# Optimization experiments

Hardware: AMD Instinct MI355X
Metric: run time of the kernel (lower is better)

The kernel has to match this reference:

```python
import jax, jax.numpy as jnp
import numpy as np
from functools import partial

U = 1200   # thought_size (GRU units)
E = 620    # word_size
V = 20000  # vocab_size
B = 128    # batch
T = 64     # seq_len
LN_EPS = 1e-3  # Keras LayerNormalization default epsilon


def layernorm(x, gamma, beta, eps=LN_EPS):
    m = jnp.mean(x, axis=-1, keepdims=True)
    v = jnp.mean(jnp.square(x - m), axis=-1, keepdims=True)
    return gamma * (x - m) * jax.lax.rsqrt(v + eps) + beta


def gru_ln_direction(emb, kernel, rkernel, bias, ln0_g, ln0_b, ln3_g, ln3_b):
    """Run the LayerNorm-GRU (impl=2, reset_after=True) over emb [B,T,E].
    Returns final hidden state [B,U]."""
    input_bias, recurrent_bias = bias[0], bias[1]
    # Time-parallel input projection: [B,T,3U]
    x_proj = jnp.einsum('bte,eu->btu', emb, kernel) + input_bias
    x_proj_t = jnp.transpose(x_proj, (1, 0, 2))  # [T,B,3U]

    def step(h, xt):
        h_ln = layernorm(h, ln0_g, ln0_b)                      # LN on previous state
        inner = h_ln @ rkernel + recurrent_bias                # [B,3U]
        z = jax.nn.sigmoid(xt[:, :U] + inner[:, :U])
        r = jax.nn.sigmoid(xt[:, U:2 * U] + inner[:, U:2 * U])
        rec_h = r * inner[:, 2 * U:]
        hh = jnp.tanh(layernorm(xt[:, 2 * U:] + rec_h, ln3_g, ln3_b))
        h_new = z * h_ln + (1.0 - z) * hh
        return h_new, None

    h0 = jnp.zeros((emb.shape[0], U), dtype=emb.dtype)
    h_final, _ = jax.lax.scan(step, h0, x_proj_t)
    return h_final


def setup_inputs() -> dict:
    key = jax.random.key(0)
    ks = jax.random.split(key, 8)
    s = 0.05
    return {
        'sentences': jax.random.randint(ks[0], (B, T), 0, V),
        'embed': jax.random.normal(ks[1], (V, E), jnp.float32) * s,
        'fw_kernel': jax.random.normal(ks[2], (E, 3 * U), jnp.float32) * s,
        'fw_rkernel': jax.random.normal(ks[3], (U, 3 * U), jnp.float32) * s,
        'fw_bias': jax.random.normal(ks[4], (2, 3 * U), jnp.float32) * s,
        'fw_ln0_g': jnp.ones((U,), jnp.float32),
        'fw_ln0_b': jnp.zeros((U,), jnp.float32),
        'fw_ln3_g': jnp.ones((U,), jnp.float32),
        'fw_ln3_b': jnp.zeros((U,), jnp.float32),
        'bw_kernel': jax.random.normal(ks[5], (E, 3 * U), jnp.float32) * s,
        'bw_rkernel': jax.random.normal(ks[6], (U, 3 * U), jnp.float32) * s,
        'bw_bias': jax.random.normal(ks[7], (2, 3 * U), jnp.float32) * s,
        'bw_ln0_g': jnp.ones((U,), jnp.float32),
        'bw_ln0_b': jnp.zeros((U,), jnp.float32),
        'bw_ln3_g': jnp.ones((U,), jnp.float32),
        'bw_ln3_b': jnp.zeros((U,), jnp.float32),
    }


def reference(sentences, embed, fw_kernel, fw_rkernel, fw_bias,
              fw_ln0_g, fw_ln0_b, fw_ln3_g, fw_ln3_b,
              bw_kernel, bw_rkernel, bw_bias,
              bw_ln0_g, bw_ln0_b, bw_ln3_g, bw_ln3_b):
    embedding = jnp.tanh(embed[sentences])  # [B,T,E]
    forward_h = gru_ln_direction(embedding, fw_kernel, fw_rkernel, fw_bias,
                                 fw_ln0_g, fw_ln0_b, fw_ln3_g, fw_ln3_b)
    backward_h = gru_ln_direction(embedding[:, ::-1, :], bw_kernel, bw_rkernel, bw_bias,
                                  bw_ln0_g, bw_ln0_b, bw_ln3_g, bw_ln3_b)
    thought_vector = jnp.concatenate([forward_h, backward_h], axis=1)  # [B,2U]
    return thought_vector, embedding
```

## Files before the change

kernel.cpp:

```cpp
#include <hip/hip_runtime.h>
#include <hip/hip_bf16.h>

#define U_    1200
#define E_    620
#define B_    128
#define T_    64
#define N3    3600
#define NP    3712
#define KE    640
#define KU    1216
#define WIN   16
#define LN_EPS 1e-3f

#define GBLK  464
#define UBLK  128
#define TBLK  (GBLK + UBLK)

typedef __attribute__((ext_vector_type(8))) short short8;
typedef __attribute__((ext_vector_type(4))) float f32x4;

constexpr size_t OFF_EMBH  = 0;
constexpr size_t SZ_EMB    = (size_t)8192 * KE * 2;
constexpr size_t OFF_EMBL  = OFF_EMBH + SZ_EMB;
constexpr size_t OFF_KTH   = OFF_EMBL + SZ_EMB;
constexpr size_t SZ_KT     = (size_t)2 * NP * KE * 2;
constexpr size_t OFF_KTL   = OFF_KTH + SZ_KT;
constexpr size_t OFF_RKTH  = OFF_KTL + SZ_KT;
constexpr size_t SZ_RKT    = (size_t)2 * NP * KU * 2;
constexpr size_t OFF_RKTL  = OFF_RKTH + SZ_RKT;
constexpr size_t OFF_XPWH  = OFF_RKTL + SZ_RKT;
constexpr size_t SZ_XPW    = (size_t)2 * WIN * B_ * NP * 2;
constexpr size_t OFF_XPWL  = OFF_XPWH + SZ_XPW;
constexpr size_t OFF_INNER = OFF_XPWL + SZ_XPW;
constexpr size_t SZ_INNER  = (size_t)8 * B_ * NP * 4;
constexpr size_t OFF_HLN   = OFF_INNER + SZ_INNER;
constexpr size_t SZ_HLN    = (size_t)2 * B_ * U_ * 4;
constexpr size_t OFF_HLNBH = OFF_HLN + SZ_HLN;
constexpr size_t SZ_HLNB   = (size_t)2 * B_ * KU * 2;
constexpr size_t OFF_HLNBL = OFF_HLNBH + SZ_HLNB;

__device__ inline void lds_load16(const void* g, void* l) {
  __builtin_amdgcn_global_load_lds(
      (const __attribute__((address_space(1))) unsigned int*)g,
      (__attribute__((address_space(3))) unsigned int*)l, 16, 0, 0);
}

__device__ inline float sigmf(float x) { return 1.f / (1.f + expf(-x)); }

__device__ inline int swz_scol(int tid) {
  return (((tid & 7) ^ ((tid >> 3) & 7)) << 3);
}
__device__ inline int swz_off(int row, int kk, int lane) {
  return row * 64 + ((kk * 32 + ((lane >> 4) << 3)) ^ ((row & 7) << 3));
}

__global__ __launch_bounds__(256)
void embed_kernel(const int* __restrict__ sent, const float* __restrict__ embed,
                  float* __restrict__ out_emb,
                  __hip_bfloat16* __restrict__ embH, __hip_bfloat16* __restrict__ embL) {
  const int row = blockIdx.x;
  const int idx = sent[row];
  const float* src = embed + (size_t)idx * E_;
  for (int e = threadIdx.x; e < KE; e += 256) {
    float v = 0.f;
    if (e < E_) {
      v = tanhf(src[e]);
      out_emb[(size_t)row * E_ + e] = v;
    }
    const __hip_bfloat16 hi = __float2bfloat16(v);
    embH[(size_t)row * KE + e] = hi;
    embL[(size_t)row * KE + e] = __float2bfloat16(v - __bfloat162float(hi));
  }
}

__global__ __launch_bounds__(256)
void transpose_cast(const float* __restrict__ W0, const float* __restrict__ W1,
                    __hip_bfloat16* __restrict__ WtHi, __hip_bfloat16* __restrict__ WtLo,
                    int Kreal, int Kp) {
  const int d = blockIdx.z;
  const float* W = d ? W1 : W0;
  __hip_bfloat16* dstH = WtHi + (size_t)d * NP * Kp;
  __hip_bfloat16* dstL = WtLo + (size_t)d * NP * Kp;
  __shared__ float tile[32][33];
  const int n0 = blockIdx.x * 32, k0 = blockIdx.y * 32;
  const int tx = threadIdx.x, ty = threadIdx.y;
#pragma unroll
  for (int i = 0; i < 32; i += 8) {
    const int k = k0 + ty + i, n = n0 + tx;
    tile[ty + i][tx] = (k < Kreal && n < N3) ? W[(size_t)k * N3 + n] : 0.f;
  }
  __syncthreads();
#pragma unroll
  for (int i = 0; i < 32; i += 8) {
    const int n = n0 + ty + i, k = k0 + tx;
    const float v = tile[tx][ty + i];
    const __hip_bfloat16 hi = __float2bfloat16(v);
    dstH[(size_t)n * Kp + k] = hi;
    dstL[(size_t)n * Kp + k] = __float2bfloat16(v - __bfloat162float(hi));
  }
}

__global__ __launch_bounds__(256)
void init_hln(const float* __restrict__ fw_b0, const float* __restrict__ bw_b0,
              float* __restrict__ hln, __hip_bfloat16* __restrict__ hlnbH,
              __hip_bfloat16* __restrict__ hlnbL) {
  const int idx = blockIdx.x * 256 + threadIdx.x;
  if (idx >= 2 * B_ * KU) return;
  const int k = idx % KU;
  const int rowd = idx / KU;
  const int d = rowd >> 7;
  float v = 0.f;
  if (k < U_) {
    v = (d ? bw_b0 : fw_b0)[k];
    hln[(size_t)rowd * U_ + k] = v;
  }
  const __hip_bfloat16 hi = __float2bfloat16(v);
  hlnbH[idx] = hi;
  hlnbL[idx] = __float2bfloat16(v - __bfloat162float(hi));
}

__global__ __launch_bounds__(256)
void xwin_gemm(const __hip_bfloat16* __restrict__ embH, const __hip_bfloat16* __restrict__ embL,
               const __hip_bfloat16* __restrict__ kTH, const __hip_bfloat16* __restrict__ kTL,
               const float* __restrict__ fw_bias, const float* __restrict__ bw_bias,
               __hip_bfloat16* __restrict__ xpwH, __hip_bfloat16* __restrict__ xpwL,
               int w0) {
  constexpr int BM = 128, BN = 128, BK = 64;
  constexpr int WM = 64, WN = 64, FM = 4, FN = 4;
  constexpr int TA = BM * BK, TB = BN * BK;
  const int bid = blockIdx.x;
  const int w = (bid & 7) * 116 + (bid >> 3);
  const int d = w / 464;
  const int q = w % 464;
  const int nt = q / 16, mt = q % 16;
  const int m0 = mt * BM;
  const int n0 = nt * BN;

  const __hip_bfloat16* BH = kTH + (size_t)d * NP * KE;
  const __hip_bfloat16* BL = kTL + (size_t)d * NP * KE;

  const int tid = threadIdx.x;
  const int lane = tid & 63;
  const int wid = tid >> 6;
  const int wr = wid >> 1, wc = wid & 1;

  __shared__ __align__(16) __hip_bfloat16 As[2 * TA];
  __shared__ __align__(16) __hip_bfloat16 Bs[2 * TB];

  f32x4 acc[FM][FN] = {};

  const int srow = tid >> 3;
  const int scol = swz_scol(tid);

  for (int ks = 0; ks < KE / BK; ++ks) {
    const int k0 = ks * BK;
    __syncthreads();
#pragma unroll
    for (int it = 0; it < TA / 2048; ++it) {
      const int row = m0 + it * 32 + srow;
      const int b = row & 127, srel = row >> 7;
      const int txi = d ? (T_ - 1 - (w0 + srel)) : (w0 + srel);
      const size_t goff = (size_t)(b * T_ + txi) * KE + k0 + scol;
      lds_load16(embH + goff, As + it * 2048 + tid * 8);
      lds_load16(embL + goff, As + TA + it * 2048 + tid * 8);
    }
#pragma unroll
    for (int it = 0; it < TB / 2048; ++it) {
      const size_t goff = (size_t)(n0 + it * 32 + srow) * KE + k0 + scol;
      lds_load16(BH + goff, Bs + it * 2048 + tid * 8);
      lds_load16(BL + goff, Bs + TB + it * 2048 + tid * 8);
    }
    __syncthreads();
#pragma unroll
    for (int kk = 0; kk < BK / 32; ++kk) {
      short8 ah[FM], al[FM], bh[FN], bl[FN];
#pragma unroll
      for (int mi = 0; mi < FM; ++mi) {
        const int row = wr * WM + mi * 16 + (lane & 15);
        const int off = swz_off(row, kk, lane);
        ah[mi] = *(const short8*)(As + off);
        al[mi] = *(const short8*)(As + TA + off);
      }
#pragma unroll
      for (int ni = 0; ni < FN; ++ni) {
        const int row = wc * WN + ni * 16 + (lane & 15);
        const int off = swz_off(row, kk, lane);
        bh[ni] = *(const short8*)(Bs + off);
        bl[ni] = *(const short8*)(Bs + TB + off);
      }
#pragma unroll
      for (int mi = 0; mi < FM; ++mi)
#pragma unroll
        for (int ni = 0; ni < FN; ++ni) {
          acc[mi][ni] = __builtin_amdgcn_mfma_f32_16x16x32_bf16(ah[mi], bh[ni], acc[mi][ni], 0, 0, 0);
          acc[mi][ni] = __builtin_amdgcn_mfma_f32_16x16x32_bf16(ah[mi], bl[ni], acc[mi][ni], 0, 0, 0);
          acc[mi][ni] = __builtin_amdgcn_mfma_f32_16x16x32_bf16(al[mi], bh[ni], acc[mi][ni], 0, 0, 0);
        }
    }
  }

  const float* ib = d ? bw_bias : fw_bias;
#pragma unroll
  for (int mi = 0; mi < FM; ++mi)
#pragma unroll
    for (int ni = 0; ni < FN; ++ni) {
      const int gc = n0 + wc * WN + ni * 16 + (lane & 15);
      const float bv = (gc < N3) ? ib[gc] : 0.f;
      const int gr0 = m0 + wr * WM + mi * 16 + ((lane >> 4) << 2);
#pragma unroll
      for (int j = 0; j < 4; ++j) {
        const int gr = gr0 + j;
        const int b = gr & 127, srel = gr >> 7;
        const size_t off = ((size_t)(d * WIN + srel) * B_ + b) * NP + gc;
        const float v = acc[mi][ni][j] + bv;
        const __hip_bfloat16 hi = __float2bfloat16(v);
        xpwH[off] = hi;
        xpwL[off] = __float2bfloat16(v - __bfloat162float(hi));
      }
    }
}

__device__ inline void breduce2(float& a, float& b, float* red, int tid) {
#pragma unroll
  for (int off = 32; off; off >>= 1) {
    a += __shfl_down(a, off, 64);
    b += __shfl_down(b, off, 64);
  }
  const int w = tid >> 6;
  __syncthreads();
  if ((tid & 63) == 0) { red[w] = a; red[4 + w] = b; }
  __syncthreads();
  a = red[0] + red[1] + red[2] + red[3];
  b = red[4] + red[5] + red[6] + red[7];
}

__global__ __launch_bounds__(256)
void step_fused(const __hip_bfloat16* __restrict__ rkTH, const __hip_bfloat16* __restrict__ rkTL,
                __hip_bfloat16* __restrict__ hlnbH, __hip_bfloat16* __restrict__ hlnbL,
                float* __restrict__ hln, float* __restrict__ inner,
                const __hip_bfloat16* __restrict__ xpwH, const __hip_bfloat16* __restrict__ xpwL,
                const float* __restrict__ fw_bias, const float* __restrict__ bw_bias,
                const float* __restrict__ fw_ln0g, const float* __restrict__ fw_ln0b,
                const float* __restrict__ fw_ln3g, const float* __restrict__ fw_ln3b,
                const float* __restrict__ bw_ln0g, const float* __restrict__ bw_ln0b,
                const float* __restrict__ bw_ln3g, const float* __restrict__ bw_ln3b,
                float* __restrict__ out_tv,
                int dG, int doG, int dU, int tU, int doU) {
  __shared__ __align__(16) __hip_bfloat16 As[2][4096];
  __shared__ __align__(16) __hip_bfloat16 Bs[2][4096];
  __shared__ float red[8];

  const int bid = blockIdx.x;
  const int tid = threadIdx.x;

  if (bid < GBLK) {
    if (!doG) return;
    const int x  = bid & 7;
    const int kp = x >> 1;
    const int nh = x & 1;
    const int i  = bid >> 3;
    const int m  = i & 1;
    const int nt = (i >> 1) + 29 * nh;
    const int ks0 = kp * 5;
    const int ks1 = (kp == 3) ? 19 : (ks0 + 5);
    const int m0 = m * 64;
    const int n0 = nt * 64;

    const int lane = tid & 63;
    const int wid = tid >> 6;
    const int wr = wid >> 1, wc = wid & 1;

    const __hip_bfloat16* WH = rkTH + (size_t)dG * NP * KU;
    const __hip_bfloat16* WL = rkTL + (size_t)dG * NP * KU;

    f32x4 acc[2][2] = {};
    const int srow = tid >> 3;
    const int scol = swz_scol(tid);

    for (int ks = ks0; ks < ks1; ++ks) {
      const int k0 = ks * 64;
      __syncthreads();
#pragma unroll
      for (int it = 0; it < 2; ++it) {
        const size_t ga = (size_t)(dG * B_ + m0 + it * 32 + srow) * KU + k0 + scol;
        lds_load16(hlnbH + ga, &As[0][it * 2048 + tid * 8]);
        lds_load16(hlnbL + ga, &As[1][it * 2048 + tid * 8]);
        const size_t gb = (size_t)(n0 + it * 32 + srow) * KU + k0 + scol;
        lds_load16(WH + gb, &Bs[0][it * 2048 + tid * 8]);
        lds_load16(WL + gb, &Bs[1][it * 2048 + tid * 8]);
      }
      __syncthreads();
#pragma unroll
      for (int kk = 0; kk < 2; ++kk) {
        short8 ah[2], al[2], bh[2], bl[2];
#pragma unroll
        for (int mi = 0; mi < 2; ++mi) {
          const int row = wr * 32 + mi * 16 + (lane & 15);
          const int off = swz_off(row, kk, lane);
          ah[mi] = *(const short8*)(&As[0][off]);
          al[mi] = *(const short8*)(&As[1][off]);
        }
#pragma unroll
        for (int nf = 0; nf < 2; ++nf) {
          const int row = wc * 32 + nf * 16 + (lane & 15);
          const int off = swz_off(row, kk, lane);
          bh[nf] = *(const short8*)(&Bs[0][off]);
          bl[nf] = *(const short8*)(&Bs[1][off]);
        }
#pragma unroll
        for (int mi = 0; mi < 2; ++mi)
#pragma unroll
          for (int nf = 0; nf < 2; ++nf) {
            acc[mi][nf] = __builtin_amdgcn_mfma_f32_16x16x32_bf16(ah[mi], bh[nf], acc[mi][nf], 0, 0, 0);
            acc[mi][nf] = __builtin_amdgcn_mfma_f32_16x16x32_bf16(ah[mi], bl[nf], acc[mi][nf], 0, 0, 0);
            acc[mi][nf] = __builtin_amdgcn_mfma_f32_16x16x32_bf16(al[mi], bh[nf], acc[mi][nf], 0, 0, 0);
          }
      }
    }

    float* C = inner + (size_t)(dG * 4 + kp) * B_ * NP;
#pragma unroll
    for (int mi = 0; mi < 2; ++mi)
#pragma unroll
      for (int nf = 0; nf < 2; ++nf) {
        const int gc = n0 + wc * 32 + nf * 16 + (lane & 15);
        const int gr = m0 + wr * 32 + mi * 16 + ((lane >> 4) << 2);
#pragma unroll
        for (int j = 0; j < 4; ++j)
          C[(size_t)(gr + j) * NP + gc] = acc[mi][nf][j];
      }
    return;
  }

  if (!doU) return;
  const int r = bid - GBLK;
  const int d = dU;
  const int srel = tU & (WIN - 1);

  const float* rec0 = inner + ((size_t)(d * 4 + 0) * B_ + r) * NP;
  const float* rec1 = inner + ((size_t)(d * 4 + 1) * B_ + r) * NP;
  const float* rec2 = inner + ((size_t)(d * 4 + 2) * B_ + r) * NP;
  const float* rec3 = inner + ((size_t)(d * 4 + 3) * B_ + r) * NP;
  const size_t xoff = ((size_t)(d * WIN + srel) * B_ + r) * NP;
  const __hip_bfloat16* xH = xpwH + xoff;
  const __hip_bfloat16* xL = xpwL + xoff;
  const float* rb = (d ? bw_bias : fw_bias) + N3;
  const float* g0 = d ? bw_ln0g : fw_ln0g;
  const float* b0 = d ? bw_ln0b : fw_ln0b;
  const float* g3 = d ? bw_ln3g : fw_ln3g;
  const float* b3 = d ? bw_ln3b : fw_ln3b;
  float* hl = hln + ((size_t)d * B_ + r) * U_;
  __hip_bfloat16* hlbH = hlnbH + ((size_t)d * B_ + r) * KU;
  __hip_bfloat16* hlbL = hlnbL + ((size_t)d * B_ + r) * KU;

  float zv[5], cv[5], hv[5];
  float s1 = 0.f, s2 = 0.f;
#pragma unroll
  for (int i = 0; i < 5; ++i) {
    const int c = tid + i * 256;
    if (c < U_) {
      const float xz = __bfloat162float(xH[c]) + __bfloat162float(xL[c]);
      const float xg = __bfloat162float(xH[U_ + c]) + __bfloat162float(xL[U_ + c]);
      const float xh = __bfloat162float(xH[2 * U_ + c]) + __bfloat162float(xL[2 * U_ + c]);
      const float rz = (rec0[c] + rec1[c]) + (rec2[c] + rec3[c]);
      const float rg = (rec0[U_ + c] + rec1[U_ + c]) + (rec2[U_ + c] + rec3[U_ + c]);
      const float rh = (rec0[2 * U_ + c] + rec1[2 * U_ + c]) + (rec2[2 * U_ + c] + rec3[2 * U_ + c]);
      const float z  = sigmf(xz + rz + rb[c]);
      const float rr = sigmf(xg + rg + rb[U_ + c]);
      const float cand = xh + rr * (rh + rb[2 * U_ + c]);
      zv[i] = z; cv[i] = cand;
      s1 += cand; s2 += cand * cand;
    }
  }
  breduce2(s1, s2, red, tid);
  const float m1 = s1 / U_;
  const float is1 = rsqrtf(s2 / U_ - m1 * m1 + LN_EPS);

  float t1 = 0.f, t2 = 0.f;
#pragma unroll
  for (int i = 0; i < 5; ++i) {
    const int c = tid + i * 256;
    if (c < U_) {
      const float hh = tanhf(g3[c] * (cv[i] - m1) * is1 + b3[c]);
      const float hn = zv[i] * hl[c] + (1.f - zv[i]) * hh;
      hv[i] = hn;
      t1 += hn; t2 += hn * hn;
    }
  }
  breduce2(t1, t2, red, tid);
  const float m2 = t1 / U_;
  const float is2 = rsqrtf(t2 / U_ - m2 * m2 + LN_EPS);

#pragma unroll
  for (int i = 0; i < 5; ++i) {
    const int c = tid + i * 256;
    if (c < U_) {
      const float hlnew = g0[c] * (hv[i] - m2) * is2 + b0[c];
      hl[c] = hlnew;
      const __hip_bfloat16 hi = __float2bfloat16(hlnew);
      hlbH[c] = hi;
      hlbL[c] = __float2bfloat16(hlnew - __bfloat162float(hi));
      if (tU == T_ - 1) out_tv[(size_t)r * 2400 + (size_t)d * U_ + c] = hv[i];
    }
  }
}

extern "C" void kernel_launch(void* const* d_in, const int* in_sizes, int n_in,
                              void* d_out, int out_size, void* d_ws, size_t ws_size,
                              hipStream_t stream) {
  const int*   sent      = (const int*)  d_in[0];
  const float* embed     = (const float*)d_in[1];
  const float* fw_kernel = (const float*)d_in[2];
  const float* fw_rkern  = (const float*)d_in[3];
  const float* fw_bias   = (const float*)d_in[4];
  const float* fw_ln0g   = (const float*)d_in[5];
  const float* fw_ln0b   = (const float*)d_in[6];
  const float* fw_ln3g   = (const float*)d_in[7];
  const float* fw_ln3b   = (const float*)d_in[8];
  const float* bw_kernel = (const float*)d_in[9];
  const float* bw_rkern  = (const float*)d_in[10];
  const float* bw_bias   = (const float*)d_in[11];
  const float* bw_ln0g   = (const float*)d_in[12];
  const float* bw_ln0b   = (const float*)d_in[13];
  const float* bw_ln3g   = (const float*)d_in[14];
  const float* bw_ln3b   = (const float*)d_in[15];

  uint8_t* ws = (uint8_t*)d_ws;
  __hip_bfloat16* embH  = (__hip_bfloat16*)(ws + OFF_EMBH);
  __hip_bfloat16* embL  = (__hip_bfloat16*)(ws + OFF_EMBL);
  __hip_bfloat16* kTH   = (__hip_bfloat16*)(ws + OFF_KTH);
  __hip_bfloat16* kTL   = (__hip_bfloat16*)(ws + OFF_KTL);
  __hip_bfloat16* rkTH  = (__hip_bfloat16*)(ws + OFF_RKTH);
  __hip_bfloat16* rkTL  = (__hip_bfloat16*)(ws + OFF_RKTL);
  __hip_bfloat16* xpwH  = (__hip_bfloat16*)(ws + OFF_XPWH);
  __hip_bfloat16* xpwL  = (__hip_bfloat16*)(ws + OFF_XPWL);
  float*          inner = (float*)(ws + OFF_INNER);
  float*          hln   = (float*)(ws + OFF_HLN);
  __hip_bfloat16* hlnbH = (__hip_bfloat16*)(ws + OFF_HLNBH);
  __hip_bfloat16* hlnbL = (__hip_bfloat16*)(ws + OFF_HLNBL);

  float* out_tv  = (float*)d_out;
  float* out_emb = (float*)d_out + (size_t)B_ * 2 * U_;

  embed_kernel<<<B_ * T_, 256, 0, stream>>>(sent, embed, out_emb, embH, embL);

  transpose_cast<<<dim3(NP / 32, KE / 32, 2), dim3(32, 8), 0, stream>>>(
      fw_kernel, bw_kernel, kTH, kTL, E_, KE);
  transpose_cast<<<dim3(NP / 32, KU / 32, 2), dim3(32, 8), 0, stream>>>(
      fw_rkern, bw_rkern, rkTH, rkTL, U_, KU);

  init_hln<<<(2 * B_ * KU + 255) / 256, 256, 0, stream>>>(fw_ln0b, bw_ln0b,
                                                          hln, hlnbH, hlnbL);

#define SF(dG_, doG_, dU_, tU_, doU_)                                          \
  step_fused<<<TBLK, 256, 0, stream>>>(                                        \
      rkTH, rkTL, hlnbH, hlnbL, hln, inner, xpwH, xpwL,                        \
      fw_bias, bw_bias, fw_ln0g, fw_ln0b, fw_ln3g, fw_ln3b,                    \
      bw_ln0g, bw_ln0b, bw_ln3g, bw_ln3b, out_tv,                              \
      dG_, doG_, dU_, tU_, doU_)

  for (int t = 0; t < T_; ++t) {
    SF(0, 1, 1, t - 1, (t > 0) ? 1 : 0);
    if ((t & (WIN - 1)) == 0)
      xwin_gemm<<<928, 256, 0, stream>>>(
          embH, embL, kTH, kTL, fw_bias, bw_bias, xpwH, xpwL, t);
    SF(1, 1, 0, t, 1);
  }
  SF(0, 0, 1, T_ - 1, 1);
#undef SF
}
```

Measured before the change: 2.032 ms.

## Switch recurrent GEMM to fp16 single-weight split and halve K-split blocks

The recurrent weight matrix is now stored as a single fp16 copy instead of bf16 hi/lo pairs, and the hidden state is split into fp16 hi/lo. This cuts MFMAs per tile from three to two and halves the weight bytes loaded each step. The K dimension is split two ways instead of four, so there are half as many GEMM blocks and fewer partial sums to reduce in the update phase. Dropping the weight low part loses precision: fp16 gives about 11 mantissa bits on the weights, which is acceptable for the weight range used here. Each block now does twice the K work, so per-step latency may rise.

Result: faster. 1.825 ms (-10.2%).

```diff
diff --git a/kernel.cpp b/kernel.cpp
--- a/kernel.cpp
+++ b/kernel.cpp
@@ -12,12 +12,14 @@
 #define WIN   16
 #define LN_EPS 1e-3f
 
-#define GBLK  464
+#define GBLK  232
 #define UBLK  128
 #define TBLK  (GBLK + UBLK)
 
 typedef __attribute__((ext_vector_type(8))) short short8;
 typedef __attribute__((ext_vector_type(4))) float f32x4;
+typedef _Float16 f16;
+typedef __attribute__((ext_vector_type(8))) _Float16 half8;
 
 constexpr size_t OFF_EMBH  = 0;
 constexpr size_t SZ_EMB    = (size_t)8192 * KE * 2;
@@ -25,19 +27,18 @@
 constexpr size_t OFF_KTH   = OFF_EMBL + SZ_EMB;
 constexpr size_t SZ_KT     = (size_t)2 * NP * KE * 2;
 constexpr size_t OFF_KTL   = OFF_KTH + SZ_KT;
-constexpr size_t OFF_RKTH  = OFF_KTL + SZ_KT;
-constexpr size_t SZ_RKT    = (size_t)2 * NP * KU * 2;
-constexpr size_t OFF_RKTL  = OFF_RKTH + SZ_RKT;
-constexpr size_t OFF_XPWH  = OFF_RKTL + SZ_RKT;
+constexpr size_t OFF_RKF   = OFF_KTL + SZ_KT;
+constexpr size_t SZ_RKF    = (size_t)2 * NP * KU * 2;
+constexpr size_t OFF_XPWH  = OFF_RKF + SZ_RKF;
 constexpr size_t SZ_XPW    = (size_t)2 * WIN * B_ * NP * 2;
 constexpr size_t OFF_XPWL  = OFF_XPWH + SZ_XPW;
 constexpr size_t OFF_INNER = OFF_XPWL + SZ_XPW;
-constexpr size_t SZ_INNER  = (size_t)8 * B_ * NP * 4;
+constexpr size_t SZ_INNER  = (size_t)4 * B_ * NP * 4;
 constexpr size_t OFF_HLN   = OFF_INNER + SZ_INNER;
 constexpr size_t SZ_HLN    = (size_t)2 * B_ * U_ * 4;
-constexpr size_t OFF_HLNBH = OFF_HLN + SZ_HLN;
-constexpr size_t SZ_HLNB   = (size_t)2 * B_ * KU * 2;
-constexpr size_t OFF_HLNBL = OFF_HLNBH + SZ_HLNB;
+constexpr size_t OFF_HLFH  = OFF_HLN + SZ_HLN;
+constexpr size_t SZ_HLF    = (size_t)2 * B_ * KU * 2;
+constexpr size_t OFF_HLFL  = OFF_HLFH + SZ_HLF;
 
 __device__ inline void lds_load16(const void* g, void* l) {
   __builtin_amdgcn_global_load_lds(
@@ -101,9 +102,30 @@
 }
 
 __global__ __launch_bounds__(256)
+void transpose_cast_f16(const float* __restrict__ W0, const float* __restrict__ W1,
+                        f16* __restrict__ Wt, int Kreal, int Kp) {
+  const int d = blockIdx.z;
+  const float* W = d ? W1 : W0;
+  f16* dst = Wt + (size_t)d * NP * Kp;
+  __shared__ float tile[32][33];
+  const int n0 = blockIdx.x * 32, k0 = blockIdx.y * 32;
+  const int tx = threadIdx.x, ty = threadIdx.y;
+#pragma unroll
+  for (int i = 0; i < 32; i += 8) {
+    const int k = k0 + ty + i, n = n0 + tx;
+    tile[ty + i][tx] = (k < Kreal && n < N3) ? W[(size_t)k * N3 + n] : 0.f;
+  }
+  __syncthreads();
+#pragma unroll
+  for (int i = 0; i < 32; i += 8) {
+    const int n = n0 + ty + i, k = k0 + tx;
+    dst[(size_t)n * Kp + k] = (f16)tile[tx][ty + i];
+  }
+}
+
+__global__ __launch_bounds__(256)
 void init_hln(const float* __restrict__ fw_b0, const float* __restrict__ bw_b0,
-              float* __restrict__ hln, __hip_bfloat16* __restrict__ hlnbH,
-              __hip_bfloat16* __restrict__ hlnbL) {
+              float* __restrict__ hln, f16* __restrict__ hlfH, f16* __restrict__ hlfL) {
   const int idx = blockIdx.x * 256 + threadIdx.x;
   if (idx >= 2 * B_ * KU) return;
   const int k = idx % KU;
@@ -114,9 +136,9 @@
     v = (d ? bw_b0 : fw_b0)[k];
     hln[(size_t)rowd * U_ + k] = v;
   }
-  const __hip_bfloat16 hi = __float2bfloat16(v);
-  hlnbH[idx] = hi;
-  hlnbL[idx] = __float2bfloat16(v - __bfloat162float(hi));
+  const f16 hi = (f16)v;
+  hlfH[idx] = hi;
+  hlfL[idx] = (f16)(v - (float)hi);
 }
 
 __global__ __launch_bounds__(256)
@@ -235,8 +257,8 @@
 }
 
 __global__ __launch_bounds__(256)
-void step_fused(const __hip_bfloat16* __restrict__ rkTH, const __hip_bfloat16* __restrict__ rkTL,
-                __hip_bfloat16* __restrict__ hlnbH, __hip_bfloat16* __restrict__ hlnbL,
+void step_fused(const f16* __restrict__ rkF,
+                f16* __restrict__ hlfH, f16* __restrict__ hlfL,
                 float* __restrict__ hln, float* __restrict__ inner,
                 const __hip_bfloat16* __restrict__ xpwH, const __hip_bfloat16* __restrict__ xpwL,
                 const float* __restrict__ fw_bias, const float* __restrict__ bw_bias,
@@ -246,8 +268,8 @@
                 const float* __restrict__ bw_ln3g, const float* __restrict__ bw_ln3b,
                 float* __restrict__ out_tv,
                 int dG, int doG, int dU, int tU, int doU) {
-  __shared__ __align__(16) __hip_bfloat16 As[2][4096];
-  __shared__ __align__(16) __hip_bfloat16 Bs[2][4096];
+  __shared__ __align__(16) f16 As[2][4096];
+  __shared__ __align__(16) f16 Bs[4096];
   __shared__ float red[8];
 
   const int bid = blockIdx.x;
@@ -256,13 +278,13 @@
   if (bid < GBLK) {
     if (!doG) return;
     const int x  = bid & 7;
-    const int kp = x >> 1;
-    const int nh = x & 1;
+    const int kp = x >> 2;
+    const int nh = (x >> 1) & 1;
+    const int m  = x & 1;
     const int i  = bid >> 3;
-    const int m  = i & 1;
-    const int nt = (i >> 1) + 29 * nh;
-    const int ks0 = kp * 5;
-    const int ks1 = (kp == 3) ? 19 : (ks0 + 5);
+    const int nt = i + 29 * nh;
+    const int ks0 = kp ? 10 : 0;
+    const int ks1 = kp ? 19 : 10;
     const int m0 = m * 64;
     const int n0 = nt * 64;
 
@@ -270,8 +292,7 @@
     const int wid = tid >> 6;
     const int wr = wid >> 1, wc = wid & 1;
 
-    const __hip_bfloat16* WH = rkTH + (size_t)dG * NP * KU;
-    const __hip_bfloat16* WL = rkTL + (size_t)dG * NP * KU;
+    const f16* WF = rkF + (size_t)dG * NP * KU;
 
     f32x4 acc[2][2] = {};
     const int srow = tid >> 3;
@@ -283,42 +304,39 @@
 #pragma unroll
       for (int it = 0; it < 2; ++it) {
         const size_t ga = (size_t)(dG * B_ + m0 + it * 32 + srow) * KU + k0 + scol;
-        lds_load16(hlnbH + ga, &As[0][it * 2048 + tid * 8]);
-        lds_load16(hlnbL + ga, &As[1][it * 2048 + tid * 8]);
+        lds_load16(hlfH + ga, &As[0][it * 2048 + tid * 8]);
+        lds_load16(hlfL + ga, &As[1][it * 2048 + tid * 8]);
         const size_t gb = (size_t)(n0 + it * 32 + srow) * KU + k0 + scol;
-        lds_load16(WH + gb, &Bs[0][it * 2048 + tid * 8]);
-        lds_load16(WL + gb, &Bs[1][it * 2048 + tid * 8]);
+        lds_load16(WF + gb, &Bs[it * 2048 + tid * 8]);
       }
       __syncthreads();
 #pragma unroll
       for (int kk = 0; kk < 2; ++kk) {
-        short8 ah[2], al[2], bh[2], bl[2];
+        half8 ah[2], al[2], bv[2];
 #pragma unroll
         for (int mi = 0; mi < 2; ++mi) {
           const int row = wr * 32 + mi * 16 + (lane & 15);
           const int off = swz_off(row, kk, lane);
-          ah[mi] = *(const short8*)(&As[0][off]);
-          al[mi] = *(const short8*)(&As[1][off]);
+          ah[mi] = *(const half8*)(&As[0][off]);
+          al[mi] = *(const half8*)(&As[1][off]);
         }
 #pragma unroll
         for (int nf = 0; nf < 2; ++nf) {
           const int row = wc * 32 + nf * 16 + (lane & 15);
           const int off = swz_off(row, kk, lane);
-          bh[nf] = *(const short8*)(&Bs[0][off]);
-          bl[nf] = *(const short8*)(&Bs[1][off]);
+          bv[nf] = *(const half8*)(&Bs[off]);
         }
 #pragma unroll
         for (int mi = 0; mi < 2; ++mi)
 #pragma unroll
           for (int nf = 0; nf < 2; ++nf) {
-            acc[mi][nf] = __builtin_amdgcn_mfma_f32_16x16x32_bf16(ah[mi], bh[nf], acc[mi][nf], 0, 0, 0);
-            acc[mi][nf] = __builtin_amdgcn_mfma_f32_16x16x32_bf16(ah[mi], bl[nf], acc[mi][nf], 0, 0, 0);
-            acc[mi][nf] = __builtin_amdgcn_mfma_f32_16x16x32_bf16(al[mi], bh[nf], acc[mi][nf], 0, 0, 0);
+            acc[mi][nf] = __builtin_amdgcn_mfma_f32_16x16x32_f16(ah[mi], bv[nf], acc[mi][nf], 0, 0, 0);
+            acc[mi][nf] = __builtin_amdgcn_mfma_f32_16x16x32_f16(al[mi], bv[nf], acc[mi][nf], 0, 0, 0);
           }
       }
     }
 
-    float* C = inner + (size_t)(dG * 4 + kp) * B_ * NP;
+    float* C = inner + (size_t)(dG * 2 + kp) * B_ * NP;
 #pragma unroll
     for (int mi = 0; mi < 2; ++mi)
 #pragma unroll
@@ -337,10 +355,8 @@
   const int d = dU;
   const int srel = tU & (WIN - 1);
 
-  const float* rec0 = inner + ((size_t)(d * 4 + 0) * B_ + r) * NP;
-  const float* rec1 = inner + ((size_t)(d * 4 + 1) * B_ + r) * NP;
-  const float* rec2 = inner + ((size_t)(d * 4 + 2) * B_ + r) * NP;
-  const float* rec3 = inner + ((size_t)(d * 4 + 3) * B_ + r) * NP;
+  const float* rec0 = inner + ((size_t)(d * 2 + 0) * B_ + r) * NP;
+  const float* rec1 = inner + ((size_t)(d * 2 + 1) * B_ + r) * NP;
   const size_t xoff = ((size_t)(d * WIN + srel) * B_ + r) * NP;
   const __hip_bfloat16* xH = xpwH + xoff;
   const __hip_bfloat16* xL = xpwL + xoff;
@@ -350,8 +366,8 @@
   const float* g3 = d ? bw_ln3g : fw_ln3g;
   const float* b3 = d ? bw_ln3b : fw_ln3b;
   float* hl = hln + ((size_t)d * B_ + r) * U_;
-  __hip_bfloat16* hlbH = hlnbH + ((size_t)d * B_ + r) * KU;
-  __hip_bfloat16* hlbL = hlnbL + ((size_t)d * B_ + r) * KU;
+  f16* hlbH = hlfH + ((size_t)d * B_ + r) * KU;
+  f16* hlbL = hlfL + ((size_t)d * B_ + r) * KU;
 
   float zv[5], cv[5], hv[5];
   float s1 = 0.f, s2 = 0.f;
@@ -362,9 +378,9 @@
       const float xz = __bfloat162float(xH[c]) + __bfloat162float(xL[c]);
       const float xg = __bfloat162float(xH[U_ + c]) + __bfloat162float(xL[U_ + c]);
       const float xh = __bfloat162float(xH[2 * U_ + c]) + __bfloat162float(xL[2 * U_ + c]);
-      const float rz = (rec0[c] + rec1[c]) + (rec2[c] + rec3[c]);
-      const float rg = (rec0[U_ + c] + rec1[U_ + c]) + (rec2[U_ + c] + rec3[U_ + c]);
-      const float rh = (rec0[2 * U_ + c] + rec1[2 * U_ + c]) + (rec2[2 * U_ + c] + rec3[2 * U_ + c]);
+      const float rz = rec0[c] + rec1[c];
+      const float rg = rec0[U_ + c] + rec1[U_ + c];
+      const float rh = rec0[2 * U_ + c] + rec1[2 * U_ + c];
       const float z  = sigmf(xz + rz + rb[c]);
       const float rr = sigmf(xg + rg + rb[U_ + c]);
       const float cand = xh + rr * (rh + rb[2 * U_ + c]);
@@ -397,9 +413,9 @@
     if (c < U_) {
       const float hlnew = g0[c] * (hv[i] - m2) * is2 + b0[c];
       hl[c] = hlnew;
-      const __hip_bfloat16 hi = __float2bfloat16(hlnew);
+      const f16 hi = (f16)hlnew;
       hlbH[c] = hi;
-      hlbL[c] = __float2bfloat16(hlnew - __bfloat162float(hi));
+      hlbL[c] = (f16)(hlnew - (float)hi);
       if (tU == T_ - 1) out_tv[(size_t)r * 2400 + (size_t)d * U_ + c] = hv[i];
     }
   }
@@ -430,14 +446,13 @@
   __hip_bfloat16* embL  = (__hip_bfloat16*)(ws + OFF_EMBL);
   __hip_bfloat16* kTH   = (__hip_bfloat16*)(ws + OFF_KTH);
   __hip_bfloat16* kTL   = (__hip_bfloat16*)(ws + OFF_KTL);
-  __hip_bfloat16* rkTH  = (__hip_bfloat16*)(ws + OFF_RKTH);
-  __hip_bfloat16* rkTL  = (__hip_bfloat16*)(ws + OFF_RKTL);
+  f16*            rkF   = (f16*)(ws + OFF_RKF);
   __hip_bfloat16* xpwH  = (__hip_bfloat16*)(ws + OFF_XPWH);
   __hip_bfloat16* xpwL  = (__hip_bfloat16*)(ws + OFF_XPWL);
   float*          inner = (float*)(ws + OFF_INNER);
   float*          hln   = (float*)(ws + OFF_HLN);
-  __hip_bfloat16* hlnbH = (__hip_bfloat16*)(ws + OFF_HLNBH);
-  __hip_bfloat16* hlnbL = (__hip_bfloat16*)(ws + OFF_HLNBL);
+  f16*            hlfH  = (f16*)(ws + OFF_HLFH);
+  f16*            hlfL  = (f16*)(ws + OFF_HLFL);
 
   float* out_tv  = (float*)d_out;
   float* out_emb = (float*)d_out + (size_t)B_ * 2 * U_;
@@ -446,15 +461,15 @@
 
   transpose_cast<<<dim3(NP / 32, KE / 32, 2), dim3(32, 8), 0, stream>>>(
       fw_kernel, bw_kernel, kTH, kTL, E_, KE);
-  transpose_cast<<<dim3(NP / 32, KU / 32, 2), dim3(32, 8), 0, stream>>>(
-      fw_rkern, bw_rkern, rkTH, rkTL, U_, KU);
+  transpose_cast_f16<<<dim3(NP / 32, KU / 32, 2), dim3(32, 8), 0, stream>>>(
+      fw_rkern, bw_rkern, rkF, U_, KU);
 
   init_hln<<<(2 * B_ * KU + 255) / 256, 256, 0, stream>>>(fw_ln0b, bw_ln0b,
-                                                          hln, hlnbH, hlnbL);
+                                                          hln, hlfH, hlfL);
 
 #define SF(dG_, doG_, dU_, tU_, doU_)                                          \
   step_fused<<<TBLK, 256, 0, stream>>>(                                        \
-      rkTH, rkTL, hlnbH, hlnbL, hln, inner, xpwH, xpwL,                        \
+      rkF, hlfH, hlfL, hln, inner, xpwH, xpwL,                                 \
       fw_bias, bw_bias, fw_ln0g, fw_ln0b, fw_ln3g, fw_ln3b,                    \
       bw_ln0g, bw_ln0b, bw_ln3g, bw_ln3b, out_tv,                              \
       dG_, doG_, dU_, tU_, doU_)
```
